# Kernel optimization log

Hardware: AMD Instinct MI355X
Metric: run time of the kernel (lower is better)

Reference implementation:

```python
import jax, jax.numpy as jnp
import numpy as np

N_NODES = 50000
IN_CH = 32
HID = 64
N_EDGES = 800000
B = 4


def setup_inputs() -> dict:
    key = jax.random.key(0)
    ks = jax.random.split(key, 20)
    inp = {
        "x": jax.random.normal(ks[0], (B, N_NODES, IN_CH), dtype=jnp.float32),
        "h": jax.random.normal(ks[1], (B, N_NODES, HID), dtype=jnp.float32),
        "edge_index": jax.random.randint(ks[2], (2, N_EDGES), 0, N_NODES, dtype=jnp.int64),
        "edge_weight": jax.random.uniform(ks[3], (N_EDGES,), dtype=jnp.float32),
    }
    # 6 GCNConv layers: uz, hz, ur, hr, uh, hh. W stored as [in, out]; bias [out].
    names = [("uz", IN_CH), ("hz", HID), ("ur", IN_CH), ("hr", HID), ("uh", IN_CH), ("hh", HID)]
    for i, (nm, cin) in enumerate(names):
        scale = 1.0 / np.sqrt(cin)
        inp[f"W_{nm}"] = jax.random.uniform(ks[4 + 2 * i], (cin, HID), minval=-scale, maxval=scale, dtype=jnp.float32)
        inp[f"b_{nm}"] = jax.random.uniform(ks[5 + 2 * i], (HID,), minval=-scale, maxval=scale, dtype=jnp.float32)
    return inp


def _gcn_norm(edge_index, edge_weight, n):
    # add self-loops with weight 1, symmetric normalization (PyG GCNConv default)
    loop = jnp.arange(n, dtype=edge_index.dtype)
    src = jnp.concatenate([edge_index[0], loop])
    dst = jnp.concatenate([edge_index[1], loop])
    w = jnp.concatenate([edge_weight, jnp.ones((n,), edge_weight.dtype)])
    deg = jnp.zeros((n,), edge_weight.dtype).at[dst].add(w)
    dinv = jnp.where(deg > 0, jax.lax.rsqrt(jnp.maximum(deg, 1e-12)), 0.0)
    norm = dinv[src] * w * dinv[dst]
    return src, dst, norm


def _gcn(x, W, b, src, dst, norm, n):
    # x: [B, N, Cin] -> [B, N, H]; linear then normalized scatter-add over edges
    xw = jnp.einsum("bnc,ch->bnh", x, W)
    msg = xw[:, src, :] * norm[None, :, None]          # [B, E+N, H]
    agg = jnp.zeros((x.shape[0], n, W.shape[1]), x.dtype).at[:, dst].add(msg)
    return agg + b


def reference(x, h, edge_index, edge_weight,
              W_uz, b_uz, W_hz, b_hz, W_ur, b_ur, W_hr, b_hr, W_uh, b_uh, W_hh, b_hh):
    n = x.shape[1]
    src, dst, norm = _gcn_norm(edge_index, edge_weight, n)
    z = jax.nn.sigmoid(_gcn(x, W_uz, b_uz, src, dst, norm, n)
                       + _gcn(h, W_hz, b_hz, src, dst, norm, n))
    r = jax.nn.sigmoid(_gcn(x, W_ur, b_ur, src, dst, norm, n)
                       + _gcn(h, W_hr, b_hr, src, dst, norm, n))
    h_hat = jnp.tanh(_gcn(x, W_uh, b_uh, src, dst, norm, n)
                     + _gcn(r * h, W_hh, b_hh, src, dst, norm, n))
    return (1.0 - z) * h + z * h_hat
```

## Files before the change

### kernel.cpp

```cpp
#include <hip/hip_runtime.h>
#include <math.h>

#define NN 50000
#define CIN 32
#define HD  64
#define NE  800000
#define NB  4
#define NBLK 196
#define NTILE 12500
#define TPB   3125
#define DWAVES 2048

typedef unsigned int uint32;
typedef unsigned short ushort_t;
typedef __attribute__((ext_vector_type(8))) short bf16x8;
typedef __attribute__((ext_vector_type(4))) float f32x4;

__device__ __forceinline__ uint32 pk2(float a, float b) {
    uint32 ua = __float_as_uint(a), ub = __float_as_uint(b);
    uint32 ra = (ua + 0x7FFFu + ((ua >> 16) & 1u)) >> 16;
    uint32 rb = (ub + 0x7FFFu + ((ub >> 16) & 1u)) >> 16;
    return ra | (rb << 16);
}
__device__ __forceinline__ ushort_t b1(float v) {
    uint32 u = __float_as_uint(v);
    return (ushort_t)((u + 0x7FFFu + ((u >> 16) & 1u)) >> 16);
}
__device__ __forceinline__ float blo(uint32 v) { return __uint_as_float(v << 16); }
__device__ __forceinline__ float bhi(uint32 v) { return __uint_as_float(v & 0xFFFF0000u); }
__device__ __forceinline__ float sigm(float v) { return 1.0f / (1.0f + __expf(-v)); }


__global__ void k_init(float* __restrict__ deg, int* __restrict__ counts) {
    int i = blockIdx.x * blockDim.x + threadIdx.x;
    if (i < NN) { deg[i] = 1.0f; counts[i] = 0; }
}

__global__ void k_pre(const float* __restrict__ x, const float* __restrict__ h,
                      const int* __restrict__ ei, const float* __restrict__ ew,
                      const float* __restrict__ Wuz, const float* __restrict__ Whz,
                      const float* __restrict__ Wur, const float* __restrict__ Whr,
                      const float* __restrict__ Wuh, const float* __restrict__ Whh,
                      const float* __restrict__ buz, const float* __restrict__ bhz,
                      const float* __restrict__ bur, const float* __restrict__ bhr,
                      const float* __restrict__ buh, const float* __restrict__ bhh,
                      uint32* __restrict__ F, float* __restrict__ deg,
                      int* __restrict__ counts,
                      uint32* __restrict__ WB, float* __restrict__ BS) {
    int stride = gridDim.x * blockDim.x;
    int tid = blockIdx.x * blockDim.x + threadIdx.x;

    if (tid < 9216) {
        int g = tid / 3072, rem = tid - g * 3072;
        int kt = rem >> 10, r2 = rem & 1023;
        int ct = r2 >> 8, r3 = r2 & 255;
        int l = r3 >> 2, jp = r3 & 3;
        int k = kt * 32 + ((l >> 4) << 3) + 2 * jp;
        int ch = ct * 16 + (l & 15);
        const float* Wu = (g == 0) ? Wuz : (g == 1) ? Wur : Wuh;
        const float* Wh = (g == 0) ? Whz : (g == 1) ? Whr : Whh;
        float w0 = (k < 32) ? Wu[k * 64 + ch] : Wh[(k - 32) * 64 + ch];
        int k1 = k + 1;
        float w1 = (k1 < 32) ? Wu[k1 * 64 + ch] : Wh[(k1 - 32) * 64 + ch];
        WB[tid] = pk2(w0, w1);
    }
    if (tid < 192) {
        int g = tid >> 6, c = tid & 63;
        const float* bu = (g == 0) ? buz : (g == 1) ? bur : buh;
        const float* bh = (g == 0) ? bhz : (g == 1) ? bhr : bhh;
        BS[tid] = bu[c] + bh[c];
    }

    for (int t = tid; t < NB * NN * (CIN / 2); t += stride) {
        int cp = t & 15; int rest = t >> 4;
        int b = rest / NN; int n = rest - b * NN;
        float2 v = *(const float2*)&x[(b * NN + n) * CIN + 2 * cp];
        F[n * 192 + b * 16 + cp] = pk2(v.x, v.y);
    }
    for (int t = tid; t < NB * NN * (HD / 2); t += stride) {
        int cp = t & 31; int rest = t >> 5;
        int b = rest / NN; int n = rest - b * NN;
        float2 v = *(const float2*)&h[(b * NN + n) * HD + 2 * cp];
        F[n * 192 + 64 + b * 32 + cp] = pk2(v.x, v.y);
    }
    for (int e = tid; e < NE; e += stride) {
        int d = ei[NE + e];
        atomicAdd(&deg[d], ew[e]);
        atomicAdd(&counts[d], 1);
    }
}


__global__ void k_scan1(const int* __restrict__ counts, int* __restrict__ tmp,
                        int* __restrict__ partials) {
    __shared__ int lds[256];
    int i = blockIdx.x * 256 + threadIdx.x;
    int v = (i < NN) ? counts[i] : 0;
    lds[threadIdx.x] = v;
    __syncthreads();
    for (int off = 1; off < 256; off <<= 1) {
        int t = (threadIdx.x >= off) ? lds[threadIdx.x - off] : 0;
        __syncthreads();
        lds[threadIdx.x] += t;
        __syncthreads();
    }
    if (i < NN) tmp[i] = lds[threadIdx.x];
    if (threadIdx.x == 255) partials[blockIdx.x] = lds[255];
}

__global__ void k_scan2(int* __restrict__ partials) {
    __shared__ int lds[256];
    int v = (threadIdx.x < NBLK) ? partials[threadIdx.x] : 0;
    lds[threadIdx.x] = v;
    __syncthreads();
    for (int off = 1; off < 256; off <<= 1) {
        int t = (threadIdx.x >= off) ? lds[threadIdx.x - off] : 0;
        __syncthreads();
        lds[threadIdx.x] += t;
        __syncthreads();
    }
    int ex = (threadIdx.x > 0) ? lds[threadIdx.x - 1] : 0;
    if (threadIdx.x < NBLK) partials[threadIdx.x] = ex;
}

__global__ void k_scan3(const int* __restrict__ tmp, const int* __restrict__ counts,
                        const int* __restrict__ partials,
                        int* __restrict__ rowptr, int* __restrict__ cursor,
                        float* __restrict__ deg) {
    int i = blockIdx.x * blockDim.x + threadIdx.x;
    if (i < NN) {
        int inc = tmp[i] + partials[i >> 8];
        rowptr[i + 1] = inc;
        cursor[i] = inc - counts[i];
        if (i == 0) rowptr[0] = 0;
        float dg = deg[i];
        deg[i] = (dg > 0.0f) ? rsqrtf(fmaxf(dg, 1e-12f)) : 0.0f;
    }
}

__global__ void k_bucket(const int* __restrict__ ei, const float* __restrict__ ew,
                         const float* __restrict__ dinv,
                         int* __restrict__ cursor, int2* __restrict__ eb) {
    int stride = gridDim.x * blockDim.x;
    for (int e = blockIdx.x * blockDim.x + threadIdx.x; e < NE; e += stride) {
        int s = ei[e], d = ei[NE + e];
        float nrm = dinv[s] * ew[e] * dinv[d];
        int pos = atomicAdd(&cursor[d], 1);
        eb[pos] = make_int2(s, __float_as_int(nrm));
    }
}


__global__ __launch_bounds__(256) void k_gather_xh(
    const int* __restrict__ rowptr, const int2* __restrict__ eb,
    const float* __restrict__ dinv, const uint32* __restrict__ F,
    uint32* __restrict__ AggU) {

    int l = threadIdx.x & 63;
    int d = __builtin_amdgcn_readfirstlane(blockIdx.x * 4 + (threadIdx.x >> 6));
    float dv = dinv[d];
    float s2 = dv * dv;

    const uint32* fp = F + 3 * l;
    const uint32* sp = fp + d * 192;
    uint32 u0 = sp[0], u1 = sp[1], u2 = sp[2];
    float a0 = s2 * blo(u0), a1 = s2 * bhi(u0);
    float a2 = s2 * blo(u1), a3 = s2 * bhi(u1);
    float a4 = s2 * blo(u2), a5 = s2 * bhi(u2);

    int e  = rowptr[d];
    int e1 = rowptr[d + 1];

    for (; e + 7 < e1; e += 8) {
        int2 p0 = eb[e],     p1 = eb[e + 1], p2 = eb[e + 2], p3 = eb[e + 3];
        int2 p4 = eb[e + 4], p5 = eb[e + 5], p6 = eb[e + 6], p7 = eb[e + 7];
        const uint32* q0 = fp + p0.x * 192;
        const uint32* q1 = fp + p1.x * 192;
        const uint32* q2 = fp + p2.x * 192;
        const uint32* q3 = fp + p3.x * 192;
        const uint32* q4 = fp + p4.x * 192;
        const uint32* q5 = fp + p5.x * 192;
        const uint32* q6 = fp + p6.x * 192;
        const uint32* q7 = fp + p7.x * 192;
        uint32 v00 = q0[0], v01 = q0[1], v02 = q0[2];
        uint32 v10 = q1[0], v11 = q1[1], v12 = q1[2];
        uint32 v20 = q2[0], v21 = q2[1], v22 = q2[2];
        uint32 v30 = q3[0], v31 = q3[1], v32 = q3[2];
        uint32 v40 = q4[0], v41 = q4[1], v42 = q4[2];
        uint32 v50 = q5[0], v51 = q5[1], v52 = q5[2];
        uint32 v60 = q6[0], v61 = q6[1], v62 = q6[2];
        uint32 v70 = q7[0], v71 = q7[1], v72 = q7[2];
        float n0 = __int_as_float(p0.y), n1 = __int_as_float(p1.y);
        float n2 = __int_as_float(p2.y), n3 = __int_as_float(p3.y);
        float n4 = __int_as_float(p4.y), n5 = __int_as_float(p5.y);
        float n6 = __int_as_float(p6.y), n7 = __int_as_float(p7.y);
        a0 = fmaf(n0, blo(v00), a0); a1 = fmaf(n0, bhi(v00), a1);
        a2 = fmaf(n0, blo(v01), a2); a3 = fmaf(n0, bhi(v01), a3);
        a4 = fmaf(n0, blo(v02), a4); a5 = fmaf(n0, bhi(v02), a5);
        a0 = fmaf(n1, blo(v10), a0); a1 = fmaf(n1, bhi(v10), a1);
        a2 = fmaf(n1, blo(v11), a2); a3 = fmaf(n1, bhi(v11), a3);
        a4 = fmaf(n1, blo(v12), a4); a5 = fmaf(n1, bhi(v12), a5);
        a0 = fmaf(n2, blo(v20), a0); a1 = fmaf(n2, bhi(v20), a1);
        a2 = fmaf(n2, blo(v21), a2); a3 = fmaf(n2, bhi(v21), a3);
        a4 = fmaf(n2, blo(v22), a4); a5 = fmaf(n2, bhi(v22), a5);
        a0 = fmaf(n3, blo(v30), a0); a1 = fmaf(n3, bhi(v30), a1);
        a2 = fmaf(n3, blo(v31), a2); a3 = fmaf(n3, bhi(v31), a3);
        a4 = fmaf(n3, blo(v32), a4); a5 = fmaf(n3, bhi(v32), a5);
        a0 = fmaf(n4, blo(v40), a0); a1 = fmaf(n4, bhi(v40), a1);
        a2 = fmaf(n4, blo(v41), a2); a3 = fmaf(n4, bhi(v41), a3);
        a4 = fmaf(n4, blo(v42), a4); a5 = fmaf(n4, bhi(v42), a5);
        a0 = fmaf(n5, blo(v50), a0); a1 = fmaf(n5, bhi(v50), a1);
        a2 = fmaf(n5, blo(v51), a2); a3 = fmaf(n5, bhi(v51), a3);
        a4 = fmaf(n5, blo(v52), a4); a5 = fmaf(n5, bhi(v52), a5);
        a0 = fmaf(n6, blo(v60), a0); a1 = fmaf(n6, bhi(v60), a1);
        a2 = fmaf(n6, blo(v61), a2); a3 = fmaf(n6, bhi(v61), a3);
        a4 = fmaf(n6, blo(v62), a4); a5 = fmaf(n6, bhi(v62), a5);
        a0 = fmaf(n7, blo(v70), a0); a1 = fmaf(n7, bhi(v70), a1);
        a2 = fmaf(n7, blo(v71), a2); a3 = fmaf(n7, bhi(v71), a3);
        a4 = fmaf(n7, blo(v72), a4); a5 = fmaf(n7, bhi(v72), a5);
    }
    for (; e + 3 < e1; e += 4) {
        int2 p0 = eb[e], p1 = eb[e + 1], p2 = eb[e + 2], p3 = eb[e + 3];
        const uint32* q0 = fp + p0.x * 192;
        const uint32* q1 = fp + p1.x * 192;
        const uint32* q2 = fp + p2.x * 192;
        const uint32* q3 = fp + p3.x * 192;
        uint32 v00 = q0[0], v01 = q0[1], v02 = q0[2];
        uint32 v10 = q1[0], v11 = q1[1], v12 = q1[2];
        uint32 v20 = q2[0], v21 = q2[1], v22 = q2[2];
        uint32 v30 = q3[0], v31 = q3[1], v32 = q3[2];
        float n0 = __int_as_float(p0.y), n1 = __int_as_float(p1.y);
        float n2 = __int_as_float(p2.y), n3 = __int_as_float(p3.y);
        a0 = fmaf(n0, blo(v00), a0); a1 = fmaf(n0, bhi(v00), a1);
        a2 = fmaf(n0, blo(v01), a2); a3 = fmaf(n0, bhi(v01), a3);
        a4 = fmaf(n0, blo(v02), a4); a5 = fmaf(n0, bhi(v02), a5);
        a0 = fmaf(n1, blo(v10), a0); a1 = fmaf(n1, bhi(v10), a1);
        a2 = fmaf(n1, blo(v11), a2); a3 = fmaf(n1, bhi(v11), a3);
        a4 = fmaf(n1, blo(v12), a4); a5 = fmaf(n1, bhi(v12), a5);
        a0 = fmaf(n2, blo(v20), a0); a1 = fmaf(n2, bhi(v20), a1);
        a2 = fmaf(n2, blo(v21), a2); a3 = fmaf(n2, bhi(v21), a3);
        a4 = fmaf(n2, blo(v22), a4); a5 = fmaf(n2, bhi(v22), a5);
        a0 = fmaf(n3, blo(v30), a0); a1 = fmaf(n3, bhi(v30), a1);
        a2 = fmaf(n3, blo(v31), a2); a3 = fmaf(n3, bhi(v31), a3);
        a4 = fmaf(n3, blo(v32), a4); a5 = fmaf(n3, bhi(v32), a5);
    }
    for (; e < e1; ++e) {
        int2 p0 = eb[e];
        const uint32* q0 = fp + p0.x * 192;
        uint32 v00 = q0[0], v01 = q0[1], v02 = q0[2];
        float n0 = __int_as_float(p0.y);
        a0 = fmaf(n0, blo(v00), a0); a1 = fmaf(n0, bhi(v00), a1);
        a2 = fmaf(n0, blo(v01), a2); a3 = fmaf(n0, bhi(v01), a3);
        a4 = fmaf(n0, blo(v02), a4); a5 = fmaf(n0, bhi(v02), a5);
    }

    uint32* op = AggU + d * 192 + 3 * l;
    op[0] = pk2(a0, a1);
    op[1] = pk2(a2, a3);
    op[2] = pk2(a4, a5);
}

__global__ __launch_bounds__(256) void k_gather_rh(
    const int* __restrict__ rowptr, const int2* __restrict__ eb,
    const float* __restrict__ dinv, const uint32* __restrict__ R,
    uint32* __restrict__ AggU) {

    int l = threadIdx.x & 63;
    int d = __builtin_amdgcn_readfirstlane(blockIdx.x * 4 + (threadIdx.x >> 6));
    float dv = dinv[d];
    float s2 = dv * dv;

    const uint32* rp = R + 2 * l;
    uint2 sv = *(const uint2*)(rp + d * 128);
    float a0 = s2 * blo(sv.x), a1 = s2 * bhi(sv.x);
    float a2 = s2 * blo(sv.y), a3 = s2 * bhi(sv.y);

    int e  = rowptr[d];
    int e1 = rowptr[d + 1];

    for (; e + 7 < e1; e += 8) {
        int2 p0 = eb[e],     p1 = eb[e + 1], p2 = eb[e + 2], p3 = eb[e + 3];
        int2 p4 = eb[e + 4], p5 = eb[e + 5], p6 = eb[e + 6], p7 = eb[e + 7];
        uint2 v0 = *(const uint2*)(rp + p0.x * 128);
        uint2 v1 = *(const uint2*)(rp + p1.x * 128);
        uint2 v2 = *(const uint2*)(rp + p2.x * 128);
        uint2 v3 = *(const uint2*)(rp + p3.x * 128);
        uint2 v4 = *(const uint2*)(rp + p4.x * 128);
        uint2 v5 = *(const uint2*)(rp + p5.x * 128);
        uint2 v6 = *(const uint2*)(rp + p6.x * 128);
        uint2 v7 = *(const uint2*)(rp + p7.x * 128);
        float n0 = __int_as_float(p0.y), n1 = __int_as_float(p1.y);
        float n2 = __int_as_float(p2.y), n3 = __int_as_float(p3.y);
        float n4 = __int_as_float(p4.y), n5 = __int_as_float(p5.y);
        float n6 = __int_as_float(p6.y), n7 = __int_as_float(p7.y);
        a0 = fmaf(n0, blo(v0.x), a0); a1 = fmaf(n0, bhi(v0.x), a1);
        a2 = fmaf(n0, blo(v0.y), a2); a3 = fmaf(n0, bhi(v0.y), a3);
        a0 = fmaf(n1, blo(v1.x), a0); a1 = fmaf(n1, bhi(v1.x), a1);
        a2 = fmaf(n1, blo(v1.y), a2); a3 = fmaf(n1, bhi(v1.y), a3);
        a0 = fmaf(n2, blo(v2.x), a0); a1 = fmaf(n2, bhi(v2.x), a1);
        a2 = fmaf(n2, blo(v2.y), a2); a3 = fmaf(n2, bhi(v2.y), a3);
        a0 = fmaf(n3, blo(v3.x), a0); a1 = fmaf(n3, bhi(v3.x), a1);
        a2 = fmaf(n3, blo(v3.y), a2); a3 = fmaf(n3, bhi(v3.y), a3);
        a0 = fmaf(n4, blo(v4.x), a0); a1 = fmaf(n4, bhi(v4.x), a1);
        a2 = fmaf(n4, blo(v4.y), a2); a3 = fmaf(n4, bhi(v4.y), a3);
        a0 = fmaf(n5, blo(v5.x), a0); a1 = fmaf(n5, bhi(v5.x), a1);
        a2 = fmaf(n5, blo(v5.y), a2); a3 = fmaf(n5, bhi(v5.y), a3);
        a0 = fmaf(n6, blo(v6.x), a0); a1 = fmaf(n6, bhi(v6.x), a1);
        a2 = fmaf(n6, blo(v6.y), a2); a3 = fmaf(n6, bhi(v6.y), a3);
        a0 = fmaf(n7, blo(v7.x), a0); a1 = fmaf(n7, bhi(v7.x), a1);
        a2 = fmaf(n7, blo(v7.y), a2); a3 = fmaf(n7, bhi(v7.y), a3);
    }
    for (; e + 3 < e1; e += 4) {
        int2 p0 = eb[e], p1 = eb[e + 1], p2 = eb[e + 2], p3 = eb[e + 3];
        uint2 v0 = *(const uint2*)(rp + p0.x * 128);
        uint2 v1 = *(const uint2*)(rp + p1.x * 128);
        uint2 v2 = *(const uint2*)(rp + p2.x * 128);
        uint2 v3 = *(const uint2*)(rp + p3.x * 128);
        float n0 = __int_as_float(p0.y), n1 = __int_as_float(p1.y);
        float n2 = __int_as_float(p2.y), n3 = __int_as_float(p3.y);
        a0 = fmaf(n0, blo(v0.x), a0); a1 = fmaf(n0, bhi(v0.x), a1);
        a2 = fmaf(n0, blo(v0.y), a2); a3 = fmaf(n0, bhi(v0.y), a3);
        a0 = fmaf(n1, blo(v1.x), a0); a1 = fmaf(n1, bhi(v1.x), a1);
        a2 = fmaf(n1, blo(v1.y), a2); a3 = fmaf(n1, bhi(v1.y), a3);
        a0 = fmaf(n2, blo(v2.x), a0); a1 = fmaf(n2, bhi(v2.x), a1);
        a2 = fmaf(n2, blo(v2.y), a2); a3 = fmaf(n2, bhi(v2.y), a3);
        a0 = fmaf(n3, blo(v3.x), a0); a1 = fmaf(n3, bhi(v3.x), a1);
        a2 = fmaf(n3, blo(v3.y), a2); a3 = fmaf(n3, bhi(v3.y), a3);
    }
    for (; e < e1; ++e) {
        int2 p0 = eb[e];
        uint2 v0 = *(const uint2*)(rp + p0.x * 128);
        float n0 = __int_as_float(p0.y);
        a0 = fmaf(n0, blo(v0.x), a0); a1 = fmaf(n0, bhi(v0.x), a1);
        a2 = fmaf(n0, blo(v0.y), a2); a3 = fmaf(n0, bhi(v0.y), a3);
    }

    *(uint2*)&AggU[d * 192 + 64 + (l >> 4) * 32 + ((2 * l) & 31)] =
        make_uint2(pk2(a0, a1), pk2(a2, a3));
}


__global__ __launch_bounds__(256) void k_zr(
    const uint32* __restrict__ AggU, const float* __restrict__ h,
    const uint32* __restrict__ WB, const float* __restrict__ BS,
    float* __restrict__ z_out, ushort_t* __restrict__ R16) {

    int l  = threadIdx.x & 63;
    int wv = blockIdx.x * 4 + (threadIdx.x >> 6);
    int lr = l & 15, lg = l >> 4;

    const bf16x8* wz = (const bf16x8*)WB;
    const bf16x8* wr = (const bf16x8*)(WB + 3072);
    bf16x8 wzf[12], wrf[12];
    #pragma unroll
    for (int f = 0; f < 12; ++f) { wzf[f] = wz[f * 64 + l]; wrf[f] = wr[f * 64 + l]; }
    float bz[4], br[4];
    #pragma unroll
    for (int ct = 0; ct < 4; ++ct) {
        bz[ct] = BS[ct * 16 + lr];
        br[ct] = BS[64 + ct * 16 + lr];
    }

    for (int t = wv; t < NTILE; t += DWAVES) {
        int bb = t / TPB, nt = t - bb * TPB;
        const uint32* base = AggU + (nt * 16 + lr) * 192;
        bf16x8 af0 = *(const bf16x8*)(base + bb * 16 + lg * 4);
        bf16x8 af1 = *(const bf16x8*)(base + 64 + bb * 32 + lg * 4);
        bf16x8 af2 = *(const bf16x8*)(base + 64 + bb * 32 + 16 + lg * 4);

        f32x4 az[4], ar[4];
        #pragma unroll
        for (int c = 0; c < 4; ++c) { az[c] = (f32x4){0,0,0,0}; ar[c] = (f32x4){0,0,0,0}; }

        #pragma unroll
        for (int ct = 0; ct < 4; ++ct) {
            az[ct] = __builtin_amdgcn_mfma_f32_16x16x32_bf16(af0, wzf[0*4+ct], az[ct], 0,0,0);
            ar[ct] = __builtin_amdgcn_mfma_f32_16x16x32_bf16(af0, wrf[0*4+ct], ar[ct], 0,0,0);
            az[ct] = __builtin_amdgcn_mfma_f32_16x16x32_bf16(af1, wzf[1*4+ct], az[ct], 0,0,0);
            ar[ct] = __builtin_amdgcn_mfma_f32_16x16x32_bf16(af1, wrf[1*4+ct], ar[ct], 0,0,0);
            az[ct] = __builtin_amdgcn_mfma_f32_16x16x32_bf16(af2, wzf[2*4+ct], az[ct], 0,0,0);
            ar[ct] = __builtin_amdgcn_mfma_f32_16x16x32_bf16(af2, wrf[2*4+ct], ar[ct], 0,0,0);
        }

        int node0 = nt * 16;
        #pragma unroll
        for (int ct = 0; ct < 4; ++ct) {
            int ch = ct * 16 + lr;
            #pragma unroll
            for (int rr = 0; rr < 4; ++rr) {
                int node = node0 + lg * 4 + rr;
                int off  = (bb * NN + node) * 64 + ch;
                float zv = sigm(az[ct][rr] + bz[ct]);
                float rv = sigm(ar[ct][rr] + br[ct]);
                float hv = h[off];
                z_out[off] = zv;
                R16[node * 256 + bb * 64 + ch] = b1(rv * hv);
            }
        }
    }
}

__global__ __launch_bounds__(256) void k_final(
    const uint32* __restrict__ AggU, const float* __restrict__ h,
    const uint32* __restrict__ WB, const float* __restrict__ BS,
    float* __restrict__ out) {

    int l  = threadIdx.x & 63;
    int wv = blockIdx.x * 4 + (threadIdx.x >> 6);
    int lr = l & 15, lg = l >> 4;

    const bf16x8* wh = (const bf16x8*)(WB + 6144);
    bf16x8 whf[12];
    #pragma unroll
    for (int f = 0; f < 12; ++f) whf[f] = wh[f * 64 + l];
    float bs[4];
    #pragma unroll
    for (int ct = 0; ct < 4; ++ct) bs[ct] = BS[128 + ct * 16 + lr];

    for (int t = wv; t < NTILE; t += DWAVES) {
        int bb = t / TPB, nt = t - bb * TPB;
        const uint32* base = AggU + (nt * 16 + lr) * 192;
        bf16x8 af0 = *(const bf16x8*)(base + bb * 16 + lg * 4);
        bf16x8 af1 = *(const bf16x8*)(base + 64 + bb * 32 + lg * 4);
        bf16x8 af2 = *(const bf16x8*)(base + 64 + bb * 32 + 16 + lg * 4);

        f32x4 ac[4];
        #pragma unroll
        for (int c = 0; c < 4; ++c) ac[c] = (f32x4){0,0,0,0};

        #pragma unroll
        for (int ct = 0; ct < 4; ++ct) {
            ac[ct] = __builtin_amdgcn_mfma_f32_16x16x32_bf16(af0, whf[0*4+ct], ac[ct], 0,0,0);
            ac[ct] = __builtin_amdgcn_mfma_f32_16x16x32_bf16(af1, whf[1*4+ct], ac[ct], 0,0,0);
            ac[ct] = __builtin_amdgcn_mfma_f32_16x16x32_bf16(af2, whf[2*4+ct], ac[ct], 0,0,0);
        }

        int node0 = nt * 16;
        #pragma unroll
        for (int ct = 0; ct < 4; ++ct) {
            int ch = ct * 16 + lr;
            #pragma unroll
            for (int rr = 0; rr < 4; ++rr) {
                int node = node0 + lg * 4 + rr;
                int off  = (bb * NN + node) * 64 + ch;
                float hh = tanhf(ac[ct][rr] + bs[ct]);
                float zv = out[off];
                float hv = h[off];
                out[off] = (1.0f - zv) * hv + zv * hh;
            }
        }
    }
}


extern "C" void kernel_launch(void* const* d_in, const int* in_sizes, int n_in,
                              void* d_out, int out_size, void* d_ws, size_t ws_size,
                              hipStream_t stream) {
    const float* x   = (const float*)d_in[0];
    const float* h   = (const float*)d_in[1];
    const int*   ei  = (const int*)d_in[2];
    const float* ew  = (const float*)d_in[3];
    const float* Wuz = (const float*)d_in[4];
    const float* buz = (const float*)d_in[5];
    const float* Whz = (const float*)d_in[6];
    const float* bhz = (const float*)d_in[7];
    const float* Wur = (const float*)d_in[8];
    const float* bur = (const float*)d_in[9];
    const float* Whr = (const float*)d_in[10];
    const float* bhr = (const float*)d_in[11];
    const float* Wuh = (const float*)d_in[12];
    const float* buh = (const float*)d_in[13];
    const float* Whh = (const float*)d_in[14];
    const float* bhh = (const float*)d_in[15];
    float* out = (float*)d_out;

    float*  w      = (float*)d_ws;
    float*  dinv   = w;
    int*    rowptr = (int*)(w + 51200);
    int2*   eb     = (int2*)(w + 102400);
    uint32* F      = (uint32*)(w + 1702400);
    uint32* R      = F;
    uint32* AggU   = (uint32*)(w + 11302400);
    uint32* WB     = (uint32*)(w + 20902400);
    float*  BS     = (float*)(w + 20911616);
    int*    counts = (int*)(w + 20911808);
    int*    tmp    = (int*)(w + 20963008);
    int*    cursor = (int*)(w + 21014208);
    int*    parts  = (int*)(w + 21065408);

    k_init<<<(NN + 255) / 256, 256, 0, stream>>>(dinv, counts);
    k_pre<<<2048, 256, 0, stream>>>(x, h, ei, ew,
                                    Wuz, Whz, Wur, Whr, Wuh, Whh,
                                    buz, bhz, bur, bhr, buh, bhh,
                                    F, dinv, counts, WB, BS);

    k_scan1<<<NBLK, 256, 0, stream>>>(counts, tmp, parts);
    k_scan2<<<1, 256, 0, stream>>>(parts);
    k_scan3<<<NBLK, 256, 0, stream>>>(tmp, counts, parts, rowptr, cursor, dinv);

    k_bucket<<<2048, 256, 0, stream>>>(ei, ew, dinv, cursor, eb);

    k_gather_xh<<<NN / 4, 256, 0, stream>>>(rowptr, eb, dinv, F, AggU);

    k_zr<<<DWAVES / 4, 256, 0, stream>>>(AggU, h, WB, BS, out, (ushort_t*)R);

    k_gather_rh<<<NN / 4, 256, 0, stream>>>(rowptr, eb, dinv, R, AggU);

    k_final<<<DWAVES / 4, 256, 0, stream>>>(AggU, h, WB, BS, out);
}
```

Baseline: 381.7 us.

## Pack degree and count into one 64-bit atomic; store z gate as bf16

Degree and in-edge count are merged into a single 64-bit fixed-point atomic per edge, replacing two separate atomics. Init is folded into the prep kernel, which removes k_init but splits the edge loop into its own kernel. The z gate is now stored as a bf16 side buffer instead of fp32 in the output, cutting write and read traffic between k_zr and k_final. The fixed-point weight sum and the bf16 z add rounding error relative to the fp32 reference.

```diff
diff --git a/kernel.cpp b/kernel.cpp
--- a/kernel.cpp
+++ b/kernel.cpp
@@ -13,6 +13,7 @@
 
 typedef unsigned int uint32;
 typedef unsigned short ushort_t;
+typedef unsigned long long u64;
 typedef __attribute__((ext_vector_type(8))) short bf16x8;
 typedef __attribute__((ext_vector_type(4))) float f32x4;
 
@@ -26,29 +27,27 @@
     uint32 u = __float_as_uint(v);
     return (ushort_t)((u + 0x7FFFu + ((u >> 16) & 1u)) >> 16);
 }
+__device__ __forceinline__ float ub(ushort_t v) {
+    return __uint_as_float(((uint32)v) << 16);
+}
 __device__ __forceinline__ float blo(uint32 v) { return __uint_as_float(v << 16); }
 __device__ __forceinline__ float bhi(uint32 v) { return __uint_as_float(v & 0xFFFF0000u); }
 __device__ __forceinline__ float sigm(float v) { return 1.0f / (1.0f + __expf(-v)); }
 
 
-__global__ void k_init(float* __restrict__ deg, int* __restrict__ counts) {
-    int i = blockIdx.x * blockDim.x + threadIdx.x;
-    if (i < NN) { deg[i] = 1.0f; counts[i] = 0; }
-}
-
-__global__ void k_pre(const float* __restrict__ x, const float* __restrict__ h,
-                      const int* __restrict__ ei, const float* __restrict__ ew,
-                      const float* __restrict__ Wuz, const float* __restrict__ Whz,
-                      const float* __restrict__ Wur, const float* __restrict__ Whr,
-                      const float* __restrict__ Wuh, const float* __restrict__ Whh,
-                      const float* __restrict__ buz, const float* __restrict__ bhz,
-                      const float* __restrict__ bur, const float* __restrict__ bhr,
-                      const float* __restrict__ buh, const float* __restrict__ bhh,
-                      uint32* __restrict__ F, float* __restrict__ deg,
-                      int* __restrict__ counts,
-                      uint32* __restrict__ WB, float* __restrict__ BS) {
+__global__ void k_prep(const float* __restrict__ x, const float* __restrict__ h,
+                       const float* __restrict__ Wuz, const float* __restrict__ Whz,
+                       const float* __restrict__ Wur, const float* __restrict__ Whr,
+                       const float* __restrict__ Wuh, const float* __restrict__ Whh,
+                       const float* __restrict__ buz, const float* __restrict__ bhz,
+                       const float* __restrict__ bur, const float* __restrict__ bhr,
+                       const float* __restrict__ buh, const float* __restrict__ bhh,
+                       uint32* __restrict__ F, u64* __restrict__ degcnt,
+                       uint32* __restrict__ WB, float* __restrict__ BS) {
     int stride = gridDim.x * blockDim.x;
     int tid = blockIdx.x * blockDim.x + threadIdx.x;
+
+    if (tid < NN) degcnt[tid] = (1ull << 24);
 
     if (tid < 9216) {
         int g = tid / 3072, rem = tid - g * 3072;
@@ -83,19 +82,24 @@
         float2 v = *(const float2*)&h[(b * NN + n) * HD + 2 * cp];
         F[n * 192 + 64 + b * 32 + cp] = pk2(v.x, v.y);
     }
-    for (int e = tid; e < NE; e += stride) {
+}
+
+__global__ void k_degcnt(const int* __restrict__ ei, const float* __restrict__ ew,
+                         u64* __restrict__ degcnt) {
+    int stride = gridDim.x * blockDim.x;
+    for (int e = blockIdx.x * blockDim.x + threadIdx.x; e < NE; e += stride) {
         int d = ei[NE + e];
-        atomicAdd(&deg[d], ew[e]);
-        atomicAdd(&counts[d], 1);
-    }
-}
-
-
-__global__ void k_scan1(const int* __restrict__ counts, int* __restrict__ tmp,
+        u64 val = (1ull << 40) + (u64)(uint32)(ew[e] * 16777216.0f + 0.5f);
+        atomicAdd(&degcnt[d], val);
+    }
+}
+
+
+__global__ void k_scan1(const u64* __restrict__ degcnt, int* __restrict__ tmp,
                         int* __restrict__ partials) {
     __shared__ int lds[256];
     int i = blockIdx.x * 256 + threadIdx.x;
-    int v = (i < NN) ? counts[i] : 0;
+    int v = (i < NN) ? (int)(degcnt[i] >> 40) : 0;
     lds[threadIdx.x] = v;
     __syncthreads();
     for (int off = 1; off < 256; off <<= 1) {
@@ -123,18 +127,20 @@
     if (threadIdx.x < NBLK) partials[threadIdx.x] = ex;
 }
 
-__global__ void k_scan3(const int* __restrict__ tmp, const int* __restrict__ counts,
+__global__ void k_scan3(const int* __restrict__ tmp, const u64* __restrict__ degcnt,
                         const int* __restrict__ partials,
                         int* __restrict__ rowptr, int* __restrict__ cursor,
-                        float* __restrict__ deg) {
+                        float* __restrict__ dinv) {
     int i = blockIdx.x * blockDim.x + threadIdx.x;
     if (i < NN) {
+        u64 dc = degcnt[i];
+        int cnt = (int)(dc >> 40);
         int inc = tmp[i] + partials[i >> 8];
         rowptr[i + 1] = inc;
-        cursor[i] = inc - counts[i];
+        cursor[i] = inc - cnt;
         if (i == 0) rowptr[0] = 0;
-        float dg = deg[i];
-        deg[i] = (dg > 0.0f) ? rsqrtf(fmaxf(dg, 1e-12f)) : 0.0f;
+        float dg = (float)(dc & 0xFFFFFFFFFFull) * 5.9604644775390625e-08f;
+        dinv[i] = (dg > 0.0f) ? rsqrtf(fmaxf(dg, 1e-12f)) : 0.0f;
     }
 }
 
@@ -343,7 +349,7 @@
 __global__ __launch_bounds__(256) void k_zr(
     const uint32* __restrict__ AggU, const float* __restrict__ h,
     const uint32* __restrict__ WB, const float* __restrict__ BS,
-    float* __restrict__ z_out, ushort_t* __restrict__ R16) {
+    ushort_t* __restrict__ Zb, ushort_t* __restrict__ R16) {
 
     int l  = threadIdx.x & 63;
     int wv = blockIdx.x * 4 + (threadIdx.x >> 6);
@@ -393,7 +399,7 @@
                 float zv = sigm(az[ct][rr] + bz[ct]);
                 float rv = sigm(ar[ct][rr] + br[ct]);
                 float hv = h[off];
-                z_out[off] = zv;
+                Zb[off] = b1(zv);
                 R16[node * 256 + bb * 64 + ch] = b1(rv * hv);
             }
         }
@@ -403,7 +409,7 @@
 __global__ __launch_bounds__(256) void k_final(
     const uint32* __restrict__ AggU, const float* __restrict__ h,
     const uint32* __restrict__ WB, const float* __restrict__ BS,
-    float* __restrict__ out) {
+    const ushort_t* __restrict__ Zb, float* __restrict__ out) {
 
     int l  = threadIdx.x & 63;
     int wv = blockIdx.x * 4 + (threadIdx.x >> 6);
@@ -444,7 +450,7 @@
                 int node = node0 + lg * 4 + rr;
                 int off  = (bb * NN + node) * 64 + ch;
                 float hh = tanhf(ac[ct][rr] + bs[ct]);
-                float zv = out[off];
+                float zv = ub(Zb[off]);
                 float hv = h[off];
                 out[off] = (1.0f - zv) * hv + zv * hh;
             }
@@ -474,37 +480,38 @@
     const float* bhh = (const float*)d_in[15];
     float* out = (float*)d_out;
 
-    float*  w      = (float*)d_ws;
-    float*  dinv   = w;
-    int*    rowptr = (int*)(w + 51200);
-    int2*   eb     = (int2*)(w + 102400);
-    uint32* F      = (uint32*)(w + 1702400);
-    uint32* R      = F;
-    uint32* AggU   = (uint32*)(w + 11302400);
-    uint32* WB     = (uint32*)(w + 20902400);
-    float*  BS     = (float*)(w + 20911616);
-    int*    counts = (int*)(w + 20911808);
-    int*    tmp    = (int*)(w + 20963008);
-    int*    cursor = (int*)(w + 21014208);
-    int*    parts  = (int*)(w + 21065408);
-
-    k_init<<<(NN + 255) / 256, 256, 0, stream>>>(dinv, counts);
-    k_pre<<<2048, 256, 0, stream>>>(x, h, ei, ew,
-                                    Wuz, Whz, Wur, Whr, Wuh, Whh,
-                                    buz, bhz, bur, bhr, buh, bhh,
-                                    F, dinv, counts, WB, BS);
-
-    k_scan1<<<NBLK, 256, 0, stream>>>(counts, tmp, parts);
+    float*    w      = (float*)d_ws;
+    u64*      degcnt = (u64*)w;
+    float*    dinv   = w + 102400;
+    int*      rowptr = (int*)(w + 153600);
+    int2*     eb     = (int2*)(w + 204800);
+    uint32*   F      = (uint32*)(w + 1804800);
+    uint32*   R      = F;
+    uint32*   AggU   = (uint32*)(w + 11404800);
+    ushort_t* Zb     = (ushort_t*)(w + 21004800);
+    uint32*   WB     = (uint32*)(w + 27404800);
+    float*    BS     = (float*)(w + 27414016);
+    int*      tmp    = (int*)(w + 27414208);
+    int*      cursor = (int*)(w + 27465408);
+    int*      parts  = (int*)(w + 27516608);
+
+    k_prep<<<2048, 256, 0, stream>>>(x, h,
+                                     Wuz, Whz, Wur, Whr, Wuh, Whh,
+                                     buz, bhz, bur, bhr, buh, bhh,
+                                     F, degcnt, WB, BS);
+    k_degcnt<<<2048, 256, 0, stream>>>(ei, ew, degcnt);
+
+    k_scan1<<<NBLK, 256, 0, stream>>>(degcnt, tmp, parts);
     k_scan2<<<1, 256, 0, stream>>>(parts);
-    k_scan3<<<NBLK, 256, 0, stream>>>(tmp, counts, parts, rowptr, cursor, dinv);
+    k_scan3<<<NBLK, 256, 0, stream>>>(tmp, degcnt, parts, rowptr, cursor, dinv);
 
     k_bucket<<<2048, 256, 0, stream>>>(ei, ew, dinv, cursor, eb);
 
     k_gather_xh<<<NN / 4, 256, 0, stream>>>(rowptr, eb, dinv, F, AggU);
 
-    k_zr<<<DWAVES / 4, 256, 0, stream>>>(AggU, h, WB, BS, out, (ushort_t*)R);
+    k_zr<<<DWAVES / 4, 256, 0, stream>>>(AggU, h, WB, BS, Zb, (ushort_t*)R);
 
     k_gather_rh<<<NN / 4, 256, 0, stream>>>(rowptr, eb, dinv, R, AggU);
 
-    k_final<<<DWAVES / 4, 256, 0, stream>>>(AggU, h, WB, BS, out);
-}
+    k_final<<<DWAVES / 4, 256, 0, stream>>>(AggU, h, WB, BS, Zb, out);
+}
```

Measured after the change: 350.7 us. 1.09x faster.
